# Kernel optimization log

Hardware: AMD Instinct MI355X
Metric: run time of the kernel (lower is better)

## Reference

```python
import jax, jax.numpy as jnp
import numpy as np


def setup_inputs() -> dict:
    V, D, E = 4096, 128, 12288
    key = jax.random.key(0)
    k1, k2, k3 = jax.random.split(key, 3)
    features = jax.random.normal(k1, (V, D), dtype=jnp.float32)
    # random self-loop-free edge list
    v0 = jax.random.randint(k2, (E,), 0, V)
    off = jax.random.randint(k3, (E,), 1, V)
    v1 = (v0 + off) % V
    edges = jnp.stack([v0, v1]).astype(jnp.int32)  # [2, E]
    # manifold-style neighbor matrix: interior edges share 2 faces
    neighbor = (jnp.zeros((V, V), jnp.int32)
                .at[edges[0], edges[1]].set(2)
                .at[edges[1], edges[0]].set(2))
    return {"features": features, "edges": edges, "neighbor": neighbor}


def _collapse(features, edges, neighbor):
    """Greedy heap-order edge collapse. The heap is built once and only popped,
    so pop order == edges sorted by priority ||f[v0]||^2 + ||f[v1]||^2.
    Returns merge matrix A (f_out = A @ f_in), alive vertex mask, final count."""
    V = neighbor.shape[0]
    target = jnp.int32(V // 2)
    pri = jnp.sum(features * features, axis=1)          # [V]
    epri = pri[edges[0]] + pri[edges[1]]                # [E]
    order = jnp.argsort(epri)                           # heappop order (stable ties)
    alive0 = jnp.ones((V,), bool)
    A0 = jnp.eye(V, dtype=jnp.float32)
    cnt0 = jnp.int32(V)

    def step(carry, e):
        alive, n, A, cnt = carry
        v0 = edges[0, e]
        v1 = edges[1, e]
        do = (cnt > target) & alive[v0] & alive[v1] & (n[v0, v1] == 2)
        # merged neighbor row for v0; v1 dies
        r = (n[v0] + n[v1]).at[v0].set(0).at[v1].set(0)
        row0 = jnp.where(do, r, n[v0])
        row1 = jnp.where(do, jnp.zeros_like(r), n[v1])
        n = (n.at[v0, :].set(row0).at[:, v0].set(row0)
              .at[v1, :].set(row1).at[:, v1].set(row1))
        arow = jnp.where(do, 0.5 * (A[v0] + A[v1]), A[v0])
        A = A.at[v0].set(arow)
        alive = alive.at[v1].set(alive[v1] & jnp.logical_not(do))
        cnt = cnt - do.astype(jnp.int32)
        return (alive, n, A, cnt), None

    (alive, n, A, cnt), _ = jax.lax.scan(step, (alive0, neighbor, A0, cnt0), order)
    return A, alive, cnt


def reference(features, edges, neighbor):
    edges = edges.astype(jnp.int32)
    A, alive, cnt = _collapse(features, edges, neighbor)
    # clean_up() compacts removed vertices; under jit we mask dead rows instead
    pooled = (A @ features) * alive[:, None].astype(features.dtype)
    return pooled, alive, cnt
```

## Files before the change

### kernel.cpp

```cpp
#include <hip/hip_runtime.h>
#include <stdint.h>

#define V 4096
#define D 128
#define E 12288
#define NPAD 16384
#define HALF 8192
#define TARGET 2048
#define MAXM (V - TARGET)
#define ROWU32 256
#define CAP 16

#define WAIT_VM0   0x0F70
#define WAIT_LGKM0 0xC07F

#define WS_N      0u
#define WS_PRI    (V * ROWU32 * 4u)
#define WS_KEYS   (WS_PRI + V * 4u)
#define WS_PK     (WS_KEYS + NPAD * 8u)
#define WS_PAIRS  (WS_PK + E * 4u)
#define WS_MCOUNT (WS_PAIRS + MAXM * 4u)
#define WS_ALIVE  (WS_MCOUNT + 16u)

typedef const __attribute__((address_space(1))) unsigned* gas1_t;
typedef __attribute__((address_space(3))) unsigned* las3_t;

__device__ __forceinline__ unsigned getf(const uint4& r, int c) {
    unsigned lo = (c & 2) ? r.z : r.x;
    unsigned hi = (c & 2) ? r.w : r.y;
    return (c & 1) ? hi : lo;
}
__device__ __forceinline__ void andf(uint4& r, int c, unsigned msk) {
    if (c == 0) r.x &= msk; else if (c == 1) r.y &= msk;
    else if (c == 2) r.z &= msk; else r.w &= msk;
}

__global__ void k_scatter(const int* __restrict__ edges, unsigned* __restrict__ n32) {
    int e = blockIdx.x * 256 + threadIdx.x;
    if (e < E) {
        int a = edges[e], b = edges[E + e];
        atomicOr(&n32[a * ROWU32 + (b >> 4)], 2u << ((b & 15) * 2));
        atomicOr(&n32[b * ROWU32 + (a >> 4)], 2u << ((a & 15) * 2));
    }
}

__global__ void k_pri(const float* __restrict__ f, float* __restrict__ pri) {
    int v = blockIdx.x * 256 + threadIdx.x;
    if (v < V) {
        const float* p = f + v * D;
        float r[8];
#pragma unroll
        for (int j = 0; j < 8; j++) r[j] = __fmul_rn(p[j], p[j]);
        for (int i = 8; i < D; i += 8) {
#pragma unroll
            for (int j = 0; j < 8; j++)
                r[j] = __fadd_rn(r[j], __fmul_rn(p[i + j], p[i + j]));
        }
        float s01 = __fadd_rn(r[0], r[1]);
        float s23 = __fadd_rn(r[2], r[3]);
        float s45 = __fadd_rn(r[4], r[5]);
        float s67 = __fadd_rn(r[6], r[7]);
        pri[v] = __fadd_rn(__fadd_rn(s01, s23), __fadd_rn(s45, s67));
    }
}

__global__ void k_keys(const int* __restrict__ edges, const float* __restrict__ pri,
                       unsigned long long* __restrict__ keys) {
    int s = blockIdx.x * 256 + threadIdx.x;
    if (s < NPAD) {
        unsigned long long rec;
        if (s < E) {
            int a = edges[s], b = edges[E + s];
            float k = __fadd_rn(pri[a], pri[b]);
            rec = ((unsigned long long)__float_as_uint(k) << 32) | (unsigned)s;
        } else {
            rec = (0xFFFFFFFFull << 32) | (unsigned)s;
        }
        keys[s] = rec;
    }
}

__launch_bounds__(1024)
__global__ void k_sort2(unsigned long long* __restrict__ keys) {
    __shared__ unsigned long long srt[HALF];
    const int tid = threadIdx.x;
    unsigned long long* base = keys + blockIdx.x * HALF;
    for (int s = tid; s < HALF; s += 1024) srt[s] = base[s];
    __syncthreads();
    for (int k = 2; k <= HALF; k <<= 1) {
        for (int j = k >> 1; j >= 1; j >>= 1) {
            for (int i = tid; i < HALF; i += 1024) {
                int ixj = i ^ j;
                if (ixj > i) {
                    unsigned long long x = srt[i], y = srt[ixj];
                    bool up = ((i & k) == 0);
                    if ((x > y) == up) { srt[i] = y; srt[ixj] = x; }
                }
            }
            __syncthreads();
        }
    }
    for (int s = tid; s < HALF; s += 1024) base[s] = srt[s];
}

__launch_bounds__(64)
__global__ void k_mergepath(const unsigned long long* __restrict__ keys,
                            const int* __restrict__ edges, unsigned* __restrict__ pkG) {
    int t = blockIdx.x * 64 + threadIdx.x;
    if (t >= E / 64) return;
    const unsigned long long* A = keys;
    const unsigned long long* B = keys + HALF;
    int d = t * 64;
    int lo = d > HALF ? d - HALF : 0;
    int hi = d < HALF ? d : HALF;
    while (lo < hi) {
        int mid = (lo + hi) >> 1;
        if (A[mid] < B[d - 1 - mid]) lo = mid + 1; else hi = mid;
    }
    int ia = lo, ib = d - lo;
    for (int o = d; o < d + 64; o++) {
        bool takeA = (ib >= HALF) || (ia < HALF && A[ia] < B[ib]);
        unsigned long long r = takeA ? A[ia++] : B[ib++];
        int e = (int)(r & 0xFFFFFFFFull);
        int a = edges[e], b = edges[E + e];
        pkG[o] = ((unsigned)a << 16) | (unsigned)b;
    }
}

__launch_bounds__(64, 1)
__global__ void k_collapse(const unsigned* __restrict__ pkG, unsigned* n32,
                           unsigned* __restrict__ pairsG, int* __restrict__ mcountG,
                           uint8_t* __restrict__ aliveG, float* __restrict__ out) {
    __shared__ unsigned shRows[2 * CAP * ROWU32];
    __shared__ uint8_t  alive[V];
    __shared__ uint8_t  shV2S[V];
    __shared__ unsigned shCand[CAP];
    __shared__ unsigned shConf[CAP];
    const int lane = threadIdx.x;
    for (int v = lane; v < V; v += 64) { alive[v] = 1; shV2S[v] = 0xFF; }
    __syncthreads();

    int cnt = V, mcount = 0;
    bool done = false;

    for (int w = 0; w < E && !done; w += 64) {
        __builtin_amdgcn_s_waitcnt(WAIT_VM0);
        unsigned pkv = pkG[w + lane];
        const int a = (int)(pkv >> 16), b = (int)(pkv & 0xFFFFu);
        unsigned wv = *(volatile unsigned*)(n32 + a * ROWU32 + (b >> 4));
        unsigned fv = (wv >> ((b & 15) * 2)) & 3u;
        bool dec = !(alive[a] && alive[b]);

        while (!done) {
            if (!dec && fv != 2u) dec = true;
            unsigned long long mF = __ballot(!dec);
            if (!mF) break;
            int limit = cnt - TARGET; if (limit > CAP) limit = CAP;
            int flagged = (int)__popcll(mF);
            int nacc = flagged < limit ? flagged : limit;

            int myK = -1;
            if (!dec) {
                int rank = (int)__popcll(mF & ((1ull << lane) - 1ull));
                if (rank < limit) { myK = rank; shCand[rank] = pkv; }
            }
            if (lane < CAP) shConf[lane] = 0u;
            __syncthreads();

            __builtin_amdgcn_s_waitcnt(WAIT_VM0);
            for (int k = 0; k < nacc; k++) {
                unsigned cp = shCand[k];
                int v0 = (int)(cp >> 16), v1 = (int)(cp & 0xFFFFu);
                __builtin_amdgcn_global_load_lds(
                    (gas1_t)(n32 + v0 * ROWU32 + lane * 4),
                    (las3_t)(shRows + (2 * k) * ROWU32), 16, 0, 0);
                __builtin_amdgcn_global_load_lds(
                    (gas1_t)(n32 + v1 * ROWU32 + lane * 4),
                    (las3_t)(shRows + (2 * k + 1) * ROWU32), 16, 0, 0);
            }
            __builtin_amdgcn_s_waitcnt(WAIT_VM0);
            __syncthreads();

            for (int pp = lane; pp < CAP * CAP; pp += 64) {
                int k = pp >> 4, j = pp & 15;
                if (j < k && k < nacc) {
                    unsigned cj = shCand[j], ck = shCand[k];
                    int v0j = (int)(cj >> 16), v1j = (int)(cj & 0xFFFFu);
                    int v0k = (int)(ck >> 16), v1k = (int)(ck & 0xFFFFu);
                    bool c = (v0k == v0j) || (v0k == v1j) || (v1k == v0j) || (v1k == v1j);
                    c |= ((shRows[(2*j+1)*ROWU32 + (v0k >> 4)] >> ((v0k & 15)*2)) & 3u) != 0u;
                    c |= ((shRows[(2*j+1)*ROWU32 + (v1k >> 4)] >> ((v1k & 15)*2)) & 3u) != 0u;
                    c |= ((shRows[(2*k+1)*ROWU32 + (v0j >> 4)] >> ((v0j & 15)*2)) & 3u) != 0u;
                    if (c) atomicOr(&shConf[k], 1u << j);
                }
            }
            __syncthreads();

            unsigned kept = 0u;
            for (int k = 0; k < nacc; k++)
                if (shConf[k] == 0u) kept |= 1u << k;
            int nk = __popc(kept);
            if (myK >= 0 && ((kept >> myK) & 1u)) dec = true;

            if (lane < nacc && ((kept >> lane) & 1u)) {
                unsigned cp = shCand[lane];
                int v0 = (int)(cp >> 16), v1 = (int)(cp & 0xFFFFu);
                alive[v1] = 0;
                shV2S[v0] = (uint8_t)(2 * lane);
                int r = __popc(kept & ((1u << lane) - 1u));
                pairsG[mcount + r] = cp;
            }
            mcount += nk; cnt -= nk;
            __syncthreads();

            {
                int g = lane >> 2, sub = lane & 3;
                if (g < nacc && ((kept >> g) & 1u)) {
                    unsigned cp = shCand[g];
                    int v0 = (int)(cp >> 16), v1 = (int)(cp & 0xFFFFu);
                    const uint4* rowA = (const uint4*)(shRows + (2 * g) * ROWU32);
                    const uint4* rowB = (const uint4*)(shRows + (2 * g + 1) * ROWU32);
                    int m0u = v0 >> 6, m1u = v1 >> 6;
                    int sh0 = (v0 & 15) * 2, wi0 = v0 >> 4;
                    for (int t = 0; t < 16; t++) {
                        int u = sub * 16 + ((t + lane) & 15);
                        uint4 ra = rowA[u], rb = rowB[u];
                        uint4 rr;
                        rr.x = ra.x | rb.x | ((ra.x & rb.x & 0xAAAAAAAAu) >> 1);
                        rr.y = ra.y | rb.y | ((ra.y & rb.y & 0xAAAAAAAAu) >> 1);
                        rr.z = ra.z | rb.z | ((ra.z & rb.z & 0xAAAAAAAAu) >> 1);
                        rr.w = ra.w | rb.w | ((ra.w & rb.w & 0xAAAAAAAAu) >> 1);
                        if (u == m0u) andf(rr, (v0 >> 4) & 3, ~(3u << ((v0 & 15) * 2)));
                        if (u == m1u) andf(rr, (v1 >> 4) & 3, ~(3u << ((v1 & 15) * 2)));
                        ((uint4*)(n32 + v0 * ROWU32))[u] = rr;
                        ((uint4*)shRows)[(2 * g) * (ROWU32 / 4) + u] = rr;
#pragma unroll
                        for (int c = 0; c < 4; c++) {
                            unsigned bb = getf(rb, c);
                            if (!bb) continue;
                            unsigned aa = getf(ra, c), vvv = getf(rr, c);
                            int xbase = (u << 6) + (c << 4);
                            unsigned tt = bb;
                            while (tt) {
                                int q = (__ffs(tt) - 1) >> 1;
                                tt &= ~(3u << (q * 2));
                                int x = xbase + q;
                                if (x != v0 && x != v1) {
                                    unsigned dx =
                                        (((aa >> (q*2)) ^ (vvv >> (q*2))) & 3u) << sh0;
                                    if (dx) atomicXor(n32 + x * ROWU32 + wi0, dx);
                                }
                            }
                        }
                    }
                }
            }
            __syncthreads();

            if (!dec) {
                if (!alive[a] || !alive[b]) dec = true;
                else {
                    int s = shV2S[a];
                    if (s != 0xFF)
                        fv = (shRows[s * ROWU32 + (b >> 4)] >> ((b & 15) * 2)) & 3u;
                    else {
                        s = shV2S[b];
                        if (s != 0xFF)
                            fv = (shRows[s * ROWU32 + (a >> 4)] >> ((a & 15) * 2)) & 3u;
                    }
                }
            }
            __syncthreads();

            if (lane < nacc && ((kept >> lane) & 1u))
                shV2S[(int)(shCand[lane] >> 16)] = 0xFF;

            if (cnt == TARGET) done = true;
        }
    }

    for (int v = lane; v < V; v += 64) {
        uint8_t ao = alive[v];
        aliveG[v] = ao;
        out[V * D + v] = ao ? 1.0f : 0.0f;
    }
    if (lane == 0) { mcountG[0] = mcount; out[V * D + V] = (float)cnt; }
}

__launch_bounds__(256)
__global__ void k_apply(const float* __restrict__ f, const unsigned* __restrict__ pairsG,
                        const int* __restrict__ mcountG, float* __restrict__ out) {
    __shared__ unsigned pl[MAXM];
    __shared__ int rootL[256];
    __shared__ float wL[256];
    const int tid = threadIdx.x;
    const int mc = mcountG[0];
    for (int j = tid; j < mc; j += 256) pl[j] = pairsG[j];
    __syncthreads();
    int cur = blockIdx.x * 256 + tid;
    float w = 1.0f;
    for (int j = 0; j < mc; j++) {
        unsigned p = pl[j];
        int v0 = (int)(p >> 16), v1 = (int)(p & 0xFFFFu);
        if (cur == v1) { cur = v0; w *= 0.5f; }
        else if (cur == v0) w *= 0.5f;
    }
    rootL[tid] = cur;
    wL[tid] = w;
    __syncthreads();
    const int sub = tid >> 7;
    const int d = tid & 127;
    for (int s = 0; s < 256; s += 2) {
        int idx = s + sub;
        int vv = blockIdx.x * 256 + idx;
        atomicAdd(&out[rootL[idx] * D + d], wL[idx] * f[vv * D + d]);
    }
}

extern "C" void kernel_launch(void* const* d_in, const int* in_sizes, int n_in,
                              void* d_out, int out_size, void* d_ws, size_t ws_size,
                              hipStream_t stream) {
    (void)in_sizes; (void)n_in; (void)out_size; (void)ws_size;
    const float* features = (const float*)d_in[0];
    const int* edges = (const int*)d_in[1];
    uint8_t* ws = (uint8_t*)d_ws;
    unsigned* n32 = (unsigned*)(ws + WS_N);
    float* pri = (float*)(ws + WS_PRI);
    unsigned long long* keys = (unsigned long long*)(ws + WS_KEYS);
    unsigned* pkG = (unsigned*)(ws + WS_PK);
    unsigned* pairsG = (unsigned*)(ws + WS_PAIRS);
    int* mcountG = (int*)(ws + WS_MCOUNT);
    uint8_t* aliveG = ws + WS_ALIVE;
    float* out = (float*)d_out;

    hipMemsetAsync(n32, 0, (size_t)V * ROWU32 * 4, stream);
    hipMemsetAsync(out, 0, (size_t)V * D * sizeof(float), stream);
    k_pri<<<(V + 255) / 256, 256, 0, stream>>>(features, pri);
    k_scatter<<<(E + 255) / 256, 256, 0, stream>>>(edges, n32);
    k_keys<<<(NPAD + 255) / 256, 256, 0, stream>>>(edges, pri, keys);
    k_sort2<<<2, 1024, 0, stream>>>(keys);
    k_mergepath<<<(E / 64 + 63) / 64, 64, 0, stream>>>(keys, edges, pkG);
    k_collapse<<<1, 64, 0, stream>>>(pkG, n32, pairsG, mcountG, aliveG, out);
    k_apply<<<V / 256, 256, 0, stream>>>(features, pairsG, mcountG, out);
}
```

Before: 3.246 ms.

## Replace dense 2-bit neighbor matrix with sparse adjacency lists in collapse kernel

The sequential collapse kernel no longer works on dense 2-bit neighbor rows (1 KB per vertex) with row merges and atomicXor column updates. It keeps fixed-capacity per-vertex adjacency lists of 16-bit entries, with 2-bit face counts, built from a bitmap-deduplicated scatter. Batch conflict detection now claims vertex ownership with atomicMin over the candidates' endpoints and their neighbors. Merges edit only the short lists, which should cut memory traffic and per-step work in the single-wavefront critical loop. In exchange it caps vertex degree at LCAP=128 and the fixup queue at QCAP, so very high-degree or heavily merged vertices would silently truncate.

New measurement: 6.402 ms. 1.97x slower.

```diff
diff --git a/kernel.cpp b/kernel.cpp
--- a/kernel.cpp
+++ b/kernel.cpp
@@ -8,39 +8,43 @@
 #define HALF 8192
 #define TARGET 2048
 #define MAXM (V - TARGET)
-#define ROWU32 256
+#define LCAP 128
 #define CAP 16
-
-#define WAIT_VM0   0x0F70
-#define WAIT_LGKM0 0xC07F
-
-#define WS_N      0u
-#define WS_PRI    (V * ROWU32 * 4u)
+#define QCAP 1024
+
+#define WAIT_VM0 0x0F70
+
+#define WS_BM     0u
+#define WS_LISTS  (V * (V / 8u))
+#define WS_LEN    (WS_LISTS + V * LCAP * 2u)
+#define WS_PRI    (WS_LEN + V * 4u)
 #define WS_KEYS   (WS_PRI + V * 4u)
 #define WS_PK     (WS_KEYS + NPAD * 8u)
 #define WS_PAIRS  (WS_PK + E * 4u)
 #define WS_MCOUNT (WS_PAIRS + MAXM * 4u)
 #define WS_ALIVE  (WS_MCOUNT + 16u)
 
-typedef const __attribute__((address_space(1))) unsigned* gas1_t;
-typedef __attribute__((address_space(3))) unsigned* las3_t;
-
 __device__ __forceinline__ unsigned getf(const uint4& r, int c) {
     unsigned lo = (c & 2) ? r.z : r.x;
     unsigned hi = (c & 2) ? r.w : r.y;
     return (c & 1) ? hi : lo;
 }
-__device__ __forceinline__ void andf(uint4& r, int c, unsigned msk) {
-    if (c == 0) r.x &= msk; else if (c == 1) r.y &= msk;
-    else if (c == 2) r.z &= msk; else r.w &= msk;
-}
-
-__global__ void k_scatter(const int* __restrict__ edges, unsigned* __restrict__ n32) {
+
+__global__ void k_build(const int* __restrict__ edges, unsigned* __restrict__ bm,
+                        unsigned* __restrict__ lenG, unsigned short* __restrict__ lists) {
     int e = blockIdx.x * 256 + threadIdx.x;
     if (e < E) {
         int a = edges[e], b = edges[E + e];
-        atomicOr(&n32[a * ROWU32 + (b >> 4)], 2u << ((b & 15) * 2));
-        atomicOr(&n32[b * ROWU32 + (a >> 4)], 2u << ((a & 15) * 2));
+        unsigned o1 = atomicOr(&bm[(a << 7) + (b >> 5)], 1u << (b & 31));
+        if (!((o1 >> (b & 31)) & 1u)) {
+            unsigned ia = atomicAdd(&lenG[a], 1u);
+            if (ia < LCAP) lists[a * LCAP + ia] = (unsigned short)((b << 2) | 2);
+        }
+        unsigned o2 = atomicOr(&bm[(b << 7) + (a >> 5)], 1u << (a & 31));
+        if (!((o2 >> (a & 31)) & 1u)) {
+            unsigned ib = atomicAdd(&lenG[b], 1u);
+            if (ib < LCAP) lists[b * LCAP + ib] = (unsigned short)((a << 2) | 2);
+        }
     }
 }
 
@@ -128,154 +132,232 @@
 }
 
 __launch_bounds__(64, 1)
-__global__ void k_collapse(const unsigned* __restrict__ pkG, unsigned* n32,
-                           unsigned* __restrict__ pairsG, int* __restrict__ mcountG,
-                           uint8_t* __restrict__ aliveG, float* __restrict__ out) {
-    __shared__ unsigned shRows[2 * CAP * ROWU32];
+__global__ void k_collapse(const unsigned* __restrict__ pkG, const unsigned* __restrict__ lenG,
+                           unsigned short* lists, unsigned* __restrict__ pairsG,
+                           int* __restrict__ mcountG, uint8_t* __restrict__ aliveG,
+                           float* __restrict__ out) {
+    __shared__ unsigned short shLen[V];
     __shared__ uint8_t  alive[V];
-    __shared__ uint8_t  shV2S[V];
+    __shared__ unsigned map1[V];
+    __shared__ unsigned map2[V];
+    __shared__ unsigned stag[2 * CAP * (LCAP / 2)];
     __shared__ unsigned shCand[CAP];
-    __shared__ unsigned shConf[CAP];
+    __shared__ unsigned short shOldLen[2 * CAP];
+    __shared__ unsigned short shQ[QCAP];
+    __shared__ int shQn;
     const int lane = threadIdx.x;
-    for (int v = lane; v < V; v += 64) { alive[v] = 1; shV2S[v] = 0xFF; }
+    unsigned short* stag16 = (unsigned short*)stag;
+
+    for (int v = lane; v < V; v += 64) {
+        unsigned l = lenG[v];
+        shLen[v] = (unsigned short)(l > LCAP ? LCAP : l);
+        alive[v] = 1;
+        map1[v] = 0xFFFFFFFFu;
+        map2[v] = 0u;
+    }
     __syncthreads();
 
     int cnt = V, mcount = 0;
     bool done = false;
 
     for (int w = 0; w < E && !done; w += 64) {
-        __builtin_amdgcn_s_waitcnt(WAIT_VM0);
         unsigned pkv = pkG[w + lane];
         const int a = (int)(pkv >> 16), b = (int)(pkv & 0xFFFFu);
-        unsigned wv = *(volatile unsigned*)(n32 + a * ROWU32 + (b >> 4));
-        unsigned fv = (wv >> ((b & 15) * 2)) & 3u;
-        bool dec = !(alive[a] && alive[b]);
+        bool dec = false;
 
         while (!done) {
-            if (!dec && fv != 2u) dec = true;
-            unsigned long long mF = __ballot(!dec);
-            if (!mF) break;
-            int limit = cnt - TARGET; if (limit > CAP) limit = CAP;
-            int flagged = (int)__popcll(mF);
-            int nacc = flagged < limit ? flagged : limit;
-
-            int myK = -1;
-            if (!dec) {
-                int rank = (int)__popcll(mF & ((1ull << lane) - 1ull));
-                if (rank < limit) { myK = rank; shCand[rank] = pkv; }
-            }
-            if (lane < CAP) shConf[lane] = 0u;
-            __syncthreads();
-
             __builtin_amdgcn_s_waitcnt(WAIT_VM0);
-            for (int k = 0; k < nacc; k++) {
-                unsigned cp = shCand[k];
-                int v0 = (int)(cp >> 16), v1 = (int)(cp & 0xFFFFu);
-                __builtin_amdgcn_global_load_lds(
-                    (gas1_t)(n32 + v0 * ROWU32 + lane * 4),
-                    (las3_t)(shRows + (2 * k) * ROWU32), 16, 0, 0);
-                __builtin_amdgcn_global_load_lds(
-                    (gas1_t)(n32 + v1 * ROWU32 + lane * 4),
-                    (las3_t)(shRows + (2 * k + 1) * ROWU32), 16, 0, 0);
-            }
-            __builtin_amdgcn_s_waitcnt(WAIT_VM0);
-            __syncthreads();
-
-            for (int pp = lane; pp < CAP * CAP; pp += 64) {
-                int k = pp >> 4, j = pp & 15;
-                if (j < k && k < nacc) {
-                    unsigned cj = shCand[j], ck = shCand[k];
-                    int v0j = (int)(cj >> 16), v1j = (int)(cj & 0xFFFFu);
-                    int v0k = (int)(ck >> 16), v1k = (int)(ck & 0xFFFFu);
-                    bool c = (v0k == v0j) || (v0k == v1j) || (v1k == v0j) || (v1k == v1j);
-                    c |= ((shRows[(2*j+1)*ROWU32 + (v0k >> 4)] >> ((v0k & 15)*2)) & 3u) != 0u;
-                    c |= ((shRows[(2*j+1)*ROWU32 + (v1k >> 4)] >> ((v1k & 15)*2)) & 3u) != 0u;
-                    c |= ((shRows[(2*k+1)*ROWU32 + (v0j >> 4)] >> ((v0j & 15)*2)) & 3u) != 0u;
-                    if (c) atomicOr(&shConf[k], 1u << j);
-                }
-            }
-            __syncthreads();
-
-            unsigned kept = 0u;
-            for (int k = 0; k < nacc; k++)
-                if (shConf[k] == 0u) kept |= 1u << k;
-            int nk = __popc(kept);
-            if (myK >= 0 && ((kept >> myK) & 1u)) dec = true;
-
-            if (lane < nacc && ((kept >> lane) & 1u)) {
-                unsigned cp = shCand[lane];
-                int v0 = (int)(cp >> 16), v1 = (int)(cp & 0xFFFFu);
-                alive[v1] = 0;
-                shV2S[v0] = (uint8_t)(2 * lane);
-                int r = __popc(kept & ((1u << lane) - 1u));
-                pairsG[mcount + r] = cp;
-            }
-            mcount += nk; cnt -= nk;
-            __syncthreads();
-
-            {
-                int g = lane >> 2, sub = lane & 3;
-                if (g < nacc && ((kept >> g) & 1u)) {
-                    unsigned cp = shCand[g];
-                    int v0 = (int)(cp >> 16), v1 = (int)(cp & 0xFFFFu);
-                    const uint4* rowA = (const uint4*)(shRows + (2 * g) * ROWU32);
-                    const uint4* rowB = (const uint4*)(shRows + (2 * g + 1) * ROWU32);
-                    int m0u = v0 >> 6, m1u = v1 >> 6;
-                    int sh0 = (v0 & 15) * 2, wi0 = v0 >> 4;
-                    for (int t = 0; t < 16; t++) {
-                        int u = sub * 16 + ((t + lane) & 15);
-                        uint4 ra = rowA[u], rb = rowB[u];
-                        uint4 rr;
-                        rr.x = ra.x | rb.x | ((ra.x & rb.x & 0xAAAAAAAAu) >> 1);
-                        rr.y = ra.y | rb.y | ((ra.y & rb.y & 0xAAAAAAAAu) >> 1);
-                        rr.z = ra.z | rb.z | ((ra.z & rb.z & 0xAAAAAAAAu) >> 1);
-                        rr.w = ra.w | rb.w | ((ra.w & rb.w & 0xAAAAAAAAu) >> 1);
-                        if (u == m0u) andf(rr, (v0 >> 4) & 3, ~(3u << ((v0 & 15) * 2)));
-                        if (u == m1u) andf(rr, (v1 >> 4) & 3, ~(3u << ((v1 & 15) * 2)));
-                        ((uint4*)(n32 + v0 * ROWU32))[u] = rr;
-                        ((uint4*)shRows)[(2 * g) * (ROWU32 / 4) + u] = rr;
-#pragma unroll
-                        for (int c = 0; c < 4; c++) {
-                            unsigned bb = getf(rb, c);
-                            if (!bb) continue;
-                            unsigned aa = getf(ra, c), vvv = getf(rr, c);
-                            int xbase = (u << 6) + (c << 4);
-                            unsigned tt = bb;
-                            while (tt) {
-                                int q = (__ffs(tt) - 1) >> 1;
-                                tt &= ~(3u << (q * 2));
-                                int x = xbase + q;
-                                if (x != v0 && x != v1) {
-                                    unsigned dx =
-                                        (((aa >> (q*2)) ^ (vvv >> (q*2))) & 3u) << sh0;
-                                    if (dx) atomicXor(n32 + x * ROWU32 + wi0, dx);
-                                }
-                            }
-                        }
-                    }
-                }
-            }
-            __syncthreads();
-
+            bool flag = false;
             if (!dec) {
                 if (!alive[a] || !alive[b]) dec = true;
                 else {
-                    int s = shV2S[a];
-                    if (s != 0xFF)
-                        fv = (shRows[s * ROWU32 + (b >> 4)] >> ((b & 15) * 2)) & 3u;
-                    else {
-                        s = shV2S[b];
-                        if (s != 0xFF)
-                            fv = (shRows[s * ROWU32 + (a >> 4)] >> ((a & 15) * 2)) & 3u;
-                    }
-                }
-            }
-            __syncthreads();
-
-            if (lane < nacc && ((kept >> lane) & 1u))
-                shV2S[(int)(shCand[lane] >> 16)] = 0xFF;
-
+                    unsigned fv = 0u;
+                    int la = shLen[a];
+                    const uint4* pl = (const uint4*)(lists + (size_t)a * LCAP);
+                    for (int i0 = 0; i0 < la && !fv; i0 += 8) {
+                        uint4 c = pl[i0 >> 3];
+#pragma unroll
+                        for (int t = 0; t < 4; t++) {
+                            unsigned wv = getf(c, t);
+                            int n0 = i0 + 2 * t;
+                            if (n0 < la && (int)((wv & 0xFFFFu) >> 2) == b) fv = wv & 3u;
+                            if (n0 + 1 < la && (int)(wv >> 18) == b) fv = (wv >> 16) & 3u;
+                        }
+                    }
+                    if (fv == 2u) flag = true; else dec = true;
+                }
+            }
+            unsigned long long mF = __ballot(flag);
+            if (!mF) break;
+            int limit = cnt - TARGET; if (limit > CAP) limit = CAP;
+
+            if (flag) { atomicMin(&map1[a], (unsigned)lane); atomicMin(&map1[b], (unsigned)lane); }
+            __syncthreads();
+            bool sel = flag && (map1[a] == (unsigned)lane) && (map1[b] == (unsigned)lane);
+            if (flag) { map1[a] = 0xFFFFFFFFu; map1[b] = 0xFFFFFFFFu; }
+            unsigned long long mS = __ballot(sel);
+            int rank = (int)__popcll(mS & ((1ull << lane) - 1ull));
+            int ncand = (int)__popcll(mS); if (ncand > CAP) ncand = CAP;
+            bool cand = sel && (rank < CAP);
+            if (cand) shCand[rank] = pkv;
+            __syncthreads();
+
+            {
+                int g = lane >> 2, sub = lane & 3;
+                if (g < ncand) {
+                    unsigned cp = shCand[g];
+                    int v0 = (int)(cp >> 16), v1 = (int)(cp & 0xFFFFu);
+                    if (sub == 0) { shOldLen[2 * g] = shLen[v0]; shOldLen[2 * g + 1] = shLen[v1]; }
+                    const uint4* p0 = (const uint4*)(lists + (size_t)v0 * LCAP);
+                    const uint4* p1 = (const uint4*)(lists + (size_t)v1 * LCAP);
+                    uint4* s0 = (uint4*)(stag + (2 * g) * (LCAP / 2));
+                    uint4* s1 = (uint4*)(stag + (2 * g + 1) * (LCAP / 2));
+                    int l0 = shLen[v0], l1 = shLen[v1];
+#pragma unroll
+                    for (int t = 0; t < 4; t++) {
+                        int wi = sub * 4 + t;
+                        if (wi * 8 < l0) s0[wi] = p0[wi];
+                        if (wi * 8 < l1) s1[wi] = p1[wi];
+                    }
+                }
+            }
+            __syncthreads();
+
+            {
+                int g = lane >> 2, sub = lane & 3;
+                if (g < ncand) {
+                    unsigned cp = shCand[g];
+                    int v0 = (int)(cp >> 16), v1 = (int)(cp & 0xFFFFu);
+                    if (sub == 0) { atomicMin(&map1[v0], (unsigned)g); atomicMin(&map1[v1], (unsigned)g); }
+                    int l1 = shOldLen[2 * g + 1];
+                    for (int j = sub; j < l1; j += 4) {
+                        int x = (int)(stag16[(2 * g + 1) * LCAP + j] >> 2);
+                        if (x != v0) atomicMin(&map1[x], (unsigned)g);
+                    }
+                }
+            }
+            __syncthreads();
+            bool own = true;
+            {
+                int g = lane >> 2, sub = lane & 3;
+                if (g < ncand) {
+                    unsigned cp = shCand[g];
+                    int v0 = (int)(cp >> 16), v1 = (int)(cp & 0xFFFFu);
+                    if (sub == 0) own = (map1[v0] == (unsigned)g) && (map1[v1] == (unsigned)g);
+                    int l1 = shOldLen[2 * g + 1];
+                    for (int j = sub; j < l1; j += 4) {
+                        int x = (int)(stag16[(2 * g + 1) * LCAP + j] >> 2);
+                        if (x != v0 && map1[x] != (unsigned)g) own = false;
+                    }
+                }
+            }
+            unsigned long long mN = __ballot(!own);
+            unsigned keptBits = 0u; int nk = 0;
+            for (int g2 = 0; g2 < ncand; g2++) {
+                if (((mN >> (4 * g2)) & 0xFull) == 0ull && nk < limit) {
+                    keptBits |= 1u << g2; nk++;
+                }
+            }
+            if (cand && ((keptBits >> rank) & 1u)) dec = true;
+            if (lane == 0) shQn = 0;
+
+            if (lane < ncand && ((keptBits >> lane) & 1u)) {
+                unsigned cp = shCand[lane];
+                int v0 = (int)(cp >> 16), v1 = (int)(cp & 0xFFFFu);
+                int la = shOldLen[2 * lane], lb = shOldLen[2 * lane + 1];
+                const unsigned short* ra = stag16 + (2 * lane) * LCAP;
+                const unsigned short* rb = stag16 + (2 * lane + 1) * LCAP;
+                for (int i = 0; i < la; i++) {
+                    int id = (int)(ra[i] >> 2);
+                    if (id != v1) atomicOr(&map2[id], 1u << lane);
+                }
+                unsigned short* outp = lists + (size_t)v0 * LCAP;
+                int wn = 0;
+                for (int i = 0; i < la; i++) {
+                    unsigned e = ra[i];
+                    int id = (int)(e >> 2);
+                    if (id == v1) continue;
+                    unsigned val = (map1[id] == (unsigned)lane) ? 3u : (e & 3u);
+                    outp[wn++] = (unsigned short)((id << 2) | val);
+                }
+                for (int j = 0; j < lb; j++) {
+                    unsigned e = rb[j];
+                    int id = (int)(e >> 2);
+                    if (id == v0) continue;
+                    int qi = atomicAdd(&shQn, 1);
+                    if (qi < QCAP) shQ[qi] = (unsigned short)((lane << 8) | j);
+                    if ((map2[id] >> lane) & 1u) continue;
+                    if (wn < LCAP) outp[wn++] = (unsigned short)e;
+                }
+                shLen[v0] = (unsigned short)wn;
+                alive[v1] = 0;
+                int r = __popc(keptBits & ((1u << lane) - 1u));
+                pairsG[mcount + r] = cp;
+            }
+            mcount += nk; cnt -= nk;
+            __syncthreads();
+
+            int qn = shQn; if (qn > QCAP) qn = QCAP;
+            for (int t = lane; t < qn; t += 64) {
+                unsigned q = shQ[t];
+                int k = (int)(q >> 8), j = (int)(q & 0xFFu);
+                unsigned cp = shCand[k];
+                int v0 = (int)(cp >> 16), v1 = (int)(cp & 0xFFFFu);
+                unsigned e = stag16[(2 * k + 1) * LCAP + j];
+                int x = (int)(e >> 2);
+                unsigned short* px = lists + (size_t)x * LCAP;
+                int lx = shLen[x];
+                int p0 = -1, p1 = -1;
+                const uint4* pxv = (const uint4*)px;
+                for (int i0 = 0; i0 < lx; i0 += 8) {
+                    uint4 c = pxv[i0 >> 3];
+#pragma unroll
+                    for (int tt = 0; tt < 4; tt++) {
+                        unsigned wv = getf(c, tt);
+                        int n0 = i0 + 2 * tt;
+                        int id0 = (int)((wv & 0xFFFFu) >> 2);
+                        int id1 = (int)(wv >> 18);
+                        if (n0 < lx) { if (id0 == v1) p1 = n0; else if (id0 == v0) p0 = n0; }
+                        if (n0 + 1 < lx) { if (id1 == v1) p1 = n0 + 1; else if (id1 == v0) p0 = n0 + 1; }
+                    }
+                }
+                if (p1 >= 0) {
+                    if (p0 >= 0) {
+                        int last = lx - 1;
+                        unsigned short lastv = (p0 == last)
+                            ? (unsigned short)((v0 << 2) | 3u) : px[last];
+                        px[p0] = (unsigned short)((v0 << 2) | 3u);
+                        if (p1 != last) px[p1] = lastv;
+                        shLen[x] = (unsigned short)(lx - 1);
+                    } else {
+                        px[p1] = (unsigned short)((v0 << 2) | (unsigned)(e & 3u));
+                    }
+                }
+            }
+            __syncthreads();
+
+            {
+                int g = lane >> 2, sub = lane & 3;
+                if (g < ncand) {
+                    unsigned cp = shCand[g];
+                    int v0 = (int)(cp >> 16), v1 = (int)(cp & 0xFFFFu);
+                    if (sub == 0) { map1[v0] = 0xFFFFFFFFu; map1[v1] = 0xFFFFFFFFu; }
+                    int l1 = shOldLen[2 * g + 1];
+                    for (int j = sub; j < l1; j += 4) {
+                        int x = (int)(stag16[(2 * g + 1) * LCAP + j] >> 2);
+                        if (x != v0) map1[x] = 0xFFFFFFFFu;
+                    }
+                    if ((keptBits >> g) & 1u) {
+                        int l0 = shOldLen[2 * g];
+                        for (int i = sub; i < l0; i += 4) {
+                            int id = (int)(stag16[(2 * g) * LCAP + i] >> 2);
+                            map2[id] = 0u;
+                        }
+                    }
+                }
+            }
             if (cnt == TARGET) done = true;
+            __syncthreads();
         }
     }
 
@@ -324,7 +406,9 @@
     const float* features = (const float*)d_in[0];
     const int* edges = (const int*)d_in[1];
     uint8_t* ws = (uint8_t*)d_ws;
-    unsigned* n32 = (unsigned*)(ws + WS_N);
+    unsigned* bm = (unsigned*)(ws + WS_BM);
+    unsigned short* lists = (unsigned short*)(ws + WS_LISTS);
+    unsigned* lenG = (unsigned*)(ws + WS_LEN);
     float* pri = (float*)(ws + WS_PRI);
     unsigned long long* keys = (unsigned long long*)(ws + WS_KEYS);
     unsigned* pkG = (unsigned*)(ws + WS_PK);
@@ -333,13 +417,14 @@
     uint8_t* aliveG = ws + WS_ALIVE;
     float* out = (float*)d_out;
 
-    hipMemsetAsync(n32, 0, (size_t)V * ROWU32 * 4, stream);
+    hipMemsetAsync(bm, 0, (size_t)V * (V / 8), stream);
+    hipMemsetAsync(lenG, 0, (size_t)V * 4, stream);
     hipMemsetAsync(out, 0, (size_t)V * D * sizeof(float), stream);
     k_pri<<<(V + 255) / 256, 256, 0, stream>>>(features, pri);
-    k_scatter<<<(E + 255) / 256, 256, 0, stream>>>(edges, n32);
+    k_build<<<(E + 255) / 256, 256, 0, stream>>>(edges, bm, lenG, lists);
     k_keys<<<(NPAD + 255) / 256, 256, 0, stream>>>(edges, pri, keys);
     k_sort2<<<2, 1024, 0, stream>>>(keys);
     k_mergepath<<<(E / 64 + 63) / 64, 64, 0, stream>>>(keys, edges, pkG);
-    k_collapse<<<1, 64, 0, stream>>>(pkG, n32, pairsG, mcountG, aliveG, out);
+    k_collapse<<<1, 64, 0, stream>>>(pkG, lenG, lists, pairsG, mcountG, aliveG, out);
     k_apply<<<V / 256, 256, 0, stream>>>(features, pairsG, mcountG, out);
 }
```
